# Kernel tuning notes

Hardware: AMD Instinct MI355X
Metric: run time of the kernel (lower is better)

## Reference

```python
import jax, jax.numpy as jnp
import numpy as np

B, T, H, L = 32, 2048, 256, 2  # batch, seq_len, hidden(=input), num_layers


def setup_inputs() -> dict:
    key = jax.random.key(0)
    k1, k2, k3 = jax.random.split(key, 3)
    x = jax.random.normal(k1, (B, T, H), dtype=jnp.float32)
    # Stacked per-layer gate weights: order (i, f, o, c_hat), Linear acts on concat([inp, h])
    bound = 1.0 / np.sqrt(2 * H)
    W = jax.random.uniform(k2, (L, 4, H, 2 * H), dtype=jnp.float32, minval=-bound, maxval=bound)
    b = jax.random.uniform(k3, (L, 4, H), dtype=jnp.float32, minval=-bound, maxval=bound)
    return {"x": x, "W": W, "b": b}


def reference(x, W, b):
    Bsz, Tlen, _ = x.shape
    nlayers, _, Hdim, _ = W.shape

    def step(carry, x_t):
        h, c = carry  # each [L, B, H]
        inp = x_t     # [B, H]
        hs, cs = [], []
        for l in range(nlayers):
            comb = jnp.concatenate([inp, h[l]], axis=-1)          # [B, 2H]
            gates = jnp.einsum('bi,ghi->bgh', comb, W[l]) + b[l]  # [B, 4, H]
            i_g = jax.nn.sigmoid(gates[:, 0])
            f_g = jax.nn.sigmoid(gates[:, 1])
            o_g = jax.nn.sigmoid(gates[:, 2])
            c_hat = jnp.tanh(gates[:, 3])
            c_new = f_g * c[l] + i_g * c_hat
            h_new = o_g * jnp.tanh(c_new)
            hs.append(h_new)
            cs.append(c_new)
            inp = h_new
        return (jnp.stack(hs), jnp.stack(cs)), inp

    h0 = jnp.zeros((nlayers, Bsz, Hdim), dtype=x.dtype)
    c0 = jnp.zeros((nlayers, Bsz, Hdim), dtype=x.dtype)
    (hT, cT), outs = jax.lax.scan(step, (h0, c0), jnp.swapaxes(x, 0, 1))
    outputs = jnp.swapaxes(outs, 0, 1)  # [B, T, H]
    return outputs, (hT[-1], cT[-1])
```

## Files before the change

kernel.cpp:

```cpp
#include <hip/hip_runtime.h>

#define BB 32
#define TT 2048
#define HH 256
#define NT 512

typedef unsigned long long ull;
typedef unsigned int uint;

__device__ __forceinline__ float sigm(float v) { return 1.0f / (1.0f + __expf(-v)); }

__device__ __forceinline__ int aload(const int* p) {
  return __hip_atomic_load(p, __ATOMIC_RELAXED, __HIP_MEMORY_SCOPE_AGENT);
}
__device__ __forceinline__ void astore(int* p, int v) {
  __hip_atomic_store(p, v, __ATOMIC_RELAXED, __HIP_MEMORY_SCOPE_AGENT);
}
__device__ __forceinline__ ull aload64(const ull* p) {
  return __hip_atomic_load(p, __ATOMIC_RELAXED, __HIP_MEMORY_SCOPE_AGENT);
}
__device__ __forceinline__ void astore64(ull* p, ull v) {
  __hip_atomic_store(p, v, __ATOMIC_RELAXED, __HIP_MEMORY_SCOPE_AGENT);
}

__global__ __launch_bounds__(NT) void lstm_scan(
    const float* __restrict__ x,
    const float* __restrict__ W,
    const float* __restrict__ bias,
    float* __restrict__ out,
    ull* __restrict__ ring,
    int* __restrict__ sync)
{
    const int bid   = blockIdx.x;
    const int c     = bid & 7;
    const int ug    = bid >> 3;
    const int layer = c >> 2;
    const int grp   = c & 3;
    const int tid   = threadIdx.x;
    const int lane  = tid & 63;
    const int wave  = tid >> 6;
    const int ks    = lane & 15;
    const int gh    = (lane >> 4) & 1;
    const int bh    = lane >> 5;
    const int col   = ug * 8 + wave;
    const int rb    = bh * 4;

    int* mOwn = sync + c * 32;
    int* mSib = sync + (4 + grp) * 32;
    ull* ringOwn = ring + (size_t)c * 8192;
    ull* ringIn  = ring + (size_t)grp * 8192;

    __shared__ float inp[8][268];
    __shared__ float hrec[8][268];

    float4 wA[8], wB[8];
    const float* WAp = W + (((size_t)layer * 4 + gh * 2)     * HH + col) * (2 * HH);
    const float* WBp = W + (((size_t)layer * 4 + gh * 2 + 1) * HH + col) * (2 * HH);
    #pragma unroll
    for (int j = 0; j < 8; ++j) {
        wA[j] = *(const float4*)(WAp + j * 64 + ks * 4);
        wB[j] = *(const float4*)(WBp + j * 64 + ks * 4);
    }

    float bb[4];
    #pragma unroll
    for (int g = 0; g < 4; ++g) bb[g] = bias[((size_t)layer * 4 + g) * HH + col];

    const int srow = tid >> 8;
    const int scol = tid & 255;

    float c_state = 0.f;

    for (int t = 0; t < TT; ++t) {
        int gv = 0x7fffffff;
        if (tid < 32)                    gv = aload(&mOwn[tid]);
        else if (layer == 0 && tid < 64) gv = aload(&mSib[tid - 32]);

        if (layer == 0) {
            #pragma unroll
            for (int j = 0; j < 4; ++j) {
                const int row = srow + 2 * j;
                inp[row][scol] = x[((size_t)(grp * 8 + row) * TT + t) * HH + scol];
            }
        } else {
            const ull* rin = ringIn + (t & 3) * 2048;
            const uint want = (uint)(t + 1);
            uint pend = 0xFu; ull v[4];
            for (;;) {
                #pragma unroll
                for (int j = 0; j < 4; ++j)
                    if (pend & (1u << j)) v[j] = aload64(&rin[tid + 512 * j]);
                #pragma unroll
                for (int j = 0; j < 4; ++j)
                    if ((pend & (1u << j)) && (uint)v[j] == want) {
                        inp[srow + 2 * j][scol] = __uint_as_float((uint)(v[j] >> 32));
                        pend &= ~(1u << j);
                    }
                if (!pend) break;
                __builtin_amdgcn_s_sleep(1);
            }
        }
        __syncthreads();

        float aA0 = 0.f, aA1 = 0.f, aA2 = 0.f, aA3 = 0.f;
        float aB0 = 0.f, aB1 = 0.f, aB2 = 0.f, aB3 = 0.f;
        #pragma unroll
        for (int j = 0; j < 4; ++j) {
            const int kof = j * 64 + ks * 4;
            float4 w0 = wA[j], w1 = wB[j];
            float4 v0 = *(const float4*)&inp[rb + 0][kof];
            float4 v1 = *(const float4*)&inp[rb + 1][kof];
            float4 v2 = *(const float4*)&inp[rb + 2][kof];
            float4 v3 = *(const float4*)&inp[rb + 3][kof];
            aA0 += v0.x * w0.x + v0.y * w0.y + v0.z * w0.z + v0.w * w0.w;
            aB0 += v0.x * w1.x + v0.y * w1.y + v0.z * w1.z + v0.w * w1.w;
            aA1 += v1.x * w0.x + v1.y * w0.y + v1.z * w0.z + v1.w * w0.w;
            aB1 += v1.x * w1.x + v1.y * w1.y + v1.z * w1.z + v1.w * w1.w;
            aA2 += v2.x * w0.x + v2.y * w0.y + v2.z * w0.z + v2.w * w0.w;
            aB2 += v2.x * w1.x + v2.y * w1.y + v2.z * w1.z + v2.w * w1.w;
            aA3 += v3.x * w0.x + v3.y * w0.y + v3.z * w0.z + v3.w * w0.w;
            aB3 += v3.x * w1.x + v3.y * w1.y + v3.z * w1.z + v3.w * w1.w;
        }

        {
            const ull* rr_ = ringOwn + ((t + 3) & 3) * 2048;
            const uint want = (uint)t;
            uint pend = 0xFu; ull v[4];
            for (;;) {
                #pragma unroll
                for (int j = 0; j < 4; ++j)
                    if (pend & (1u << j)) v[j] = aload64(&rr_[tid + 512 * j]);
                #pragma unroll
                for (int j = 0; j < 4; ++j)
                    if ((pend & (1u << j)) && (uint)v[j] == want) {
                        hrec[srow + 2 * j][scol] = __uint_as_float((uint)(v[j] >> 32));
                        pend &= ~(1u << j);
                    }
                if (!pend) break;
                __builtin_amdgcn_s_sleep(1);
            }
        }
        if (tid < 32) {
            while (gv < t - 2) { __builtin_amdgcn_s_sleep(1); gv = aload(&mOwn[tid]); }
        } else if (layer == 0 && tid < 64) {
            while (gv < t - 3) { __builtin_amdgcn_s_sleep(1); gv = aload(&mSib[tid - 32]); }
        }
        __syncthreads();
        if (tid == 0) astore(&mOwn[ug], t + 1);

        #pragma unroll
        for (int j = 4; j < 8; ++j) {
            const int kof = (j - 4) * 64 + ks * 4;
            float4 w0 = wA[j], w1 = wB[j];
            float4 v0 = *(const float4*)&hrec[rb + 0][kof];
            float4 v1 = *(const float4*)&hrec[rb + 1][kof];
            float4 v2 = *(const float4*)&hrec[rb + 2][kof];
            float4 v3 = *(const float4*)&hrec[rb + 3][kof];
            aA0 += v0.x * w0.x + v0.y * w0.y + v0.z * w0.z + v0.w * w0.w;
            aB0 += v0.x * w1.x + v0.y * w1.y + v0.z * w1.z + v0.w * w1.w;
            aA1 += v1.x * w0.x + v1.y * w0.y + v1.z * w0.z + v1.w * w0.w;
            aB1 += v1.x * w1.x + v1.y * w1.y + v1.z * w1.z + v1.w * w1.w;
            aA2 += v2.x * w0.x + v2.y * w0.y + v2.z * w0.z + v2.w * w0.w;
            aB2 += v2.x * w1.x + v2.y * w1.y + v2.z * w1.z + v2.w * w1.w;
            aA3 += v3.x * w0.x + v3.y * w0.y + v3.z * w0.z + v3.w * w0.w;
            aB3 += v3.x * w1.x + v3.y * w1.y + v3.z * w1.z + v3.w * w1.w;
        }

        #pragma unroll
        for (int m = 1; m <= 8; m <<= 1) {
            aA0 += __shfl_xor(aA0, m);
            aA1 += __shfl_xor(aA1, m);
            aA2 += __shfl_xor(aA2, m);
            aA3 += __shfl_xor(aA3, m);
            aB0 += __shfl_xor(aB0, m);
            aB1 += __shfl_xor(aB1, m);
            aB2 += __shfl_xor(aB2, m);
            aB3 += __shfl_xor(aB3, m);
        }
        float oA0 = __shfl_xor(aA0, 16), oA1 = __shfl_xor(aA1, 16);
        float oA2 = __shfl_xor(aA2, 16), oA3 = __shfl_xor(aA3, 16);
        float qB0 = __shfl_xor(aB0, 16), qB1 = __shfl_xor(aB1, 16);
        float qB2 = __shfl_xor(aB2, 16), qB3 = __shfl_xor(aB3, 16);

        if (gh == 0 && ks < 4) {
            const int bl = rb + ks;
            float iv = ks == 0 ? aA0 : ks == 1 ? aA1 : ks == 2 ? aA2 : aA3;
            float fv = ks == 0 ? aB0 : ks == 1 ? aB1 : ks == 2 ? aB2 : aB3;
            float ov = ks == 0 ? oA0 : ks == 1 ? oA1 : ks == 2 ? oA2 : oA3;
            float qv = ks == 0 ? qB0 : ks == 1 ? qB1 : ks == 2 ? qB2 : qB3;
            float ig = sigm(iv + bb[0]);
            float fg = sigm(fv + bb[1]);
            float og = sigm(ov + bb[2]);
            float ch = tanhf(qv + bb[3]);
            c_state = fg * c_state + ig * ch;
            float hn = og * tanhf(c_state);
            astore64(&ringOwn[(t & 3) * 2048 + bl * 256 + col],
                     ((ull)__float_as_uint(hn) << 32) | (ull)(uint)(t + 1));
            if (layer == 1) {
                const int bglob = grp * 8 + bl;
                out[((size_t)bglob * TT + t) * HH + col] = hn;
                if (t == TT - 1) {
                    float* tail = out + (size_t)BB * TT * HH;
                    tail[bglob * HH + col] = hn;
                    tail[BB * HH + bglob * HH + col] = c_state;
                }
            }
        }
        __syncthreads();
    }
}

extern "C" void kernel_launch(void* const* d_in, const int* in_sizes, int n_in,
                              void* d_out, int out_size, void* d_ws, size_t ws_size,
                              hipStream_t stream) {
    (void)in_sizes; (void)n_in; (void)out_size; (void)ws_size;
    const float* x    = (const float*)d_in[0];
    const float* W    = (const float*)d_in[1];
    const float* bias = (const float*)d_in[2];
    float* out  = (float*)d_out;
    int*   sync = (int*)d_ws;
    ull*   ring = (ull*)((char*)d_ws + 4096);

    hipMemsetAsync(d_ws, 0, 4096 + 8 * 8192 * sizeof(ull), stream);
    hipLaunchKernelGGL(lstm_scan, dim3(256), dim3(NT), 0, stream, x, W, bias, out, ring, sync);
}
```

Before: 7.131 ms.

## Double-buffer LDS inputs, prefetch x into registers, drop trailing barrier

Double-buffers the shared-memory input and recurrent-state tiles by step parity, which lets the end-of-step __syncthreads be removed. Layer-0 blocks prefetch the next step's x values into registers so the global load latency overlaps the current step. The spin-wait loops now poll a few times before sleeping, to cut wake-up latency on the cross-block handoff. This saves one barrier per step and hides load latency, in exchange for more LDS use and more polling traffic on the ring buffers.

```diff
diff --git a/kernel.cpp b/kernel.cpp
--- a/kernel.cpp
+++ b/kernel.cpp
@@ -50,8 +50,8 @@
     ull* ringOwn = ring + (size_t)c * 8192;
     ull* ringIn  = ring + (size_t)grp * 8192;
 
-    __shared__ float inp[8][268];
-    __shared__ float hrec[8][268];
+    __shared__ float inp[2][8][268];
+    __shared__ float hrec[2][8][268];
 
     float4 wA[8], wB[8];
     const float* WAp = W + (((size_t)layer * 4 + gh * 2)     * HH + col) * (2 * HH);
@@ -69,23 +69,38 @@
     const int srow = tid >> 8;
     const int scol = tid & 255;
 
+    float xr0 = 0.f, xr1 = 0.f, xr2 = 0.f, xr3 = 0.f;
+    if (layer == 0) {
+        const float* xb = x + (size_t)(grp * 8 + srow) * TT * HH + scol;
+        xr0 = xb[0 * 2 * TT * HH];
+        xr1 = xb[1 * 2 * TT * HH];
+        xr2 = xb[2 * 2 * TT * HH];
+        xr3 = xb[3 * 2 * TT * HH];
+    }
+
     float c_state = 0.f;
 
     for (int t = 0; t < TT; ++t) {
+        const int p = t & 1;
         int gv = 0x7fffffff;
         if (tid < 32)                    gv = aload(&mOwn[tid]);
         else if (layer == 0 && tid < 64) gv = aload(&mSib[tid - 32]);
 
         if (layer == 0) {
-            #pragma unroll
-            for (int j = 0; j < 4; ++j) {
-                const int row = srow + 2 * j;
-                inp[row][scol] = x[((size_t)(grp * 8 + row) * TT + t) * HH + scol];
-            }
+            inp[p][srow + 0][scol] = xr0;
+            inp[p][srow + 2][scol] = xr1;
+            inp[p][srow + 4][scol] = xr2;
+            inp[p][srow + 6][scol] = xr3;
+            const int tn = (t + 1 < TT) ? t + 1 : t;
+            const float* xb = x + ((size_t)(grp * 8 + srow) * TT + tn) * HH + scol;
+            xr0 = xb[0 * 2 * TT * HH];
+            xr1 = xb[1 * 2 * TT * HH];
+            xr2 = xb[2 * 2 * TT * HH];
+            xr3 = xb[3 * 2 * TT * HH];
         } else {
             const ull* rin = ringIn + (t & 3) * 2048;
             const uint want = (uint)(t + 1);
-            uint pend = 0xFu; ull v[4];
+            uint pend = 0xFu; ull v[4]; int tries = 0;
             for (;;) {
                 #pragma unroll
                 for (int j = 0; j < 4; ++j)
@@ -93,11 +108,11 @@
                 #pragma unroll
                 for (int j = 0; j < 4; ++j)
                     if ((pend & (1u << j)) && (uint)v[j] == want) {
-                        inp[srow + 2 * j][scol] = __uint_as_float((uint)(v[j] >> 32));
+                        inp[p][srow + 2 * j][scol] = __uint_as_float((uint)(v[j] >> 32));
                         pend &= ~(1u << j);
                     }
                 if (!pend) break;
-                __builtin_amdgcn_s_sleep(1);
+                if (++tries > 4) __builtin_amdgcn_s_sleep(1);
             }
         }
         __syncthreads();
@@ -108,10 +123,10 @@
         for (int j = 0; j < 4; ++j) {
             const int kof = j * 64 + ks * 4;
             float4 w0 = wA[j], w1 = wB[j];
-            float4 v0 = *(const float4*)&inp[rb + 0][kof];
-            float4 v1 = *(const float4*)&inp[rb + 1][kof];
-            float4 v2 = *(const float4*)&inp[rb + 2][kof];
-            float4 v3 = *(const float4*)&inp[rb + 3][kof];
+            float4 v0 = *(const float4*)&inp[p][rb + 0][kof];
+            float4 v1 = *(const float4*)&inp[p][rb + 1][kof];
+            float4 v2 = *(const float4*)&inp[p][rb + 2][kof];
+            float4 v3 = *(const float4*)&inp[p][rb + 3][kof];
             aA0 += v0.x * w0.x + v0.y * w0.y + v0.z * w0.z + v0.w * w0.w;
             aB0 += v0.x * w1.x + v0.y * w1.y + v0.z * w1.z + v0.w * w1.w;
             aA1 += v1.x * w0.x + v1.y * w0.y + v1.z * w0.z + v1.w * w0.w;
@@ -125,7 +140,7 @@
         {
             const ull* rr_ = ringOwn + ((t + 3) & 3) * 2048;
             const uint want = (uint)t;
-            uint pend = 0xFu; ull v[4];
+            uint pend = 0xFu; ull v[4]; int tries = 0;
             for (;;) {
                 #pragma unroll
                 for (int j = 0; j < 4; ++j)
@@ -133,11 +148,11 @@
                 #pragma unroll
                 for (int j = 0; j < 4; ++j)
                     if ((pend & (1u << j)) && (uint)v[j] == want) {
-                        hrec[srow + 2 * j][scol] = __uint_as_float((uint)(v[j] >> 32));
+                        hrec[p][srow + 2 * j][scol] = __uint_as_float((uint)(v[j] >> 32));
                         pend &= ~(1u << j);
                     }
                 if (!pend) break;
-                __builtin_amdgcn_s_sleep(1);
+                if (++tries > 4) __builtin_amdgcn_s_sleep(1);
             }
         }
         if (tid < 32) {
@@ -152,10 +167,10 @@
         for (int j = 4; j < 8; ++j) {
             const int kof = (j - 4) * 64 + ks * 4;
             float4 w0 = wA[j], w1 = wB[j];
-            float4 v0 = *(const float4*)&hrec[rb + 0][kof];
-            float4 v1 = *(const float4*)&hrec[rb + 1][kof];
-            float4 v2 = *(const float4*)&hrec[rb + 2][kof];
-            float4 v3 = *(const float4*)&hrec[rb + 3][kof];
+            float4 v0 = *(const float4*)&hrec[p][rb + 0][kof];
+            float4 v1 = *(const float4*)&hrec[p][rb + 1][kof];
+            float4 v2 = *(const float4*)&hrec[p][rb + 2][kof];
+            float4 v3 = *(const float4*)&hrec[p][rb + 3][kof];
             aA0 += v0.x * w0.x + v0.y * w0.y + v0.z * w0.z + v0.w * w0.w;
             aB0 += v0.x * w1.x + v0.y * w1.y + v0.z * w1.z + v0.w * w1.w;
             aA1 += v1.x * w0.x + v1.y * w0.y + v1.z * w0.z + v1.w * w0.w;
@@ -206,7 +221,6 @@
                 }
             }
         }
-        __syncthreads();
     }
 }
 
```

New measurement: 6.401 ms. -10.2%, faster.
